# Optimization experiments

Measured on AMD Instinct MI355X. Metric: run time of the kernel, lower is better.

## Reference

```python
import jax, jax.numpy as jnp
import numpy as np

B, M, N, C = 1, 128, 256, 256
MID, OUT_C = 32, 128
LN_EPS = 1e-5
NORM_EPS = 1e-3


def setup_inputs() -> dict:
    key = jax.random.key(0)
    ks = jax.random.split(key, 9)
    act = jax.random.normal(ks[0], (B, M, N, C), dtype=jnp.float32)
    mask = (jax.random.uniform(ks[1], (B, M, N)) < 0.9).astype(jnp.float32)
    s_in = 1.0 / np.sqrt(C)
    s_mid = 1.0 / np.sqrt(MID * MID)
    return {
        "act": act,
        "mask": mask,
        "ln_g": jnp.ones((C,), jnp.float32),
        "ln_b": jnp.zeros((C,), jnp.float32),
        "lw": jax.random.normal(ks[2], (MID, C), jnp.float32) * s_in,
        "lb": jnp.zeros((MID,), jnp.float32),
        "rw": jax.random.normal(ks[3], (MID, C), jnp.float32) * s_in,
        "rb": jnp.zeros((MID,), jnp.float32),
        "ow": jax.random.normal(ks[4], (OUT_C, MID * MID), jnp.float32) * s_mid,
        "ob": jnp.zeros((OUT_C,), jnp.float32),
    }


def reference(act, mask, ln_g, ln_b, lw, lb, rw, rb, ow, ob):
    # LayerNorm over channel dim
    mu = jnp.mean(act, axis=-1, keepdims=True)
    var = jnp.mean(jnp.square(act - mu), axis=-1, keepdims=True)
    x = (act - mu) * jax.lax.rsqrt(var + LN_EPS) * ln_g + ln_b  # [b,m,i,c]

    m = mask[..., None]  # [b,m,i,1]
    left = m * (jnp.einsum('bmic,xc->bmix', x, lw) + lb)   # [b,m,i,mid]
    right = m * (jnp.einsum('bmic,yc->bmiy', x, rw) + rb)  # [b,m,i,mid]

    # outer product mean over MSA dim m -> [b,i,j,x,y]
    x2d = jnp.einsum('bmix,bmjy->bijxy', left, right)
    x2d = x2d.reshape(x2d.shape[:3] + (MID * MID,))
    out = jnp.einsum('bijk,ok->bijo', x2d, ow) + ob  # [b,i,j,out_c]

    norm = jnp.einsum('bmi,bmj->bij', mask, mask)[..., None]
    return out / (norm + NORM_EPS)
```

## Files before the change

kernel.cpp:

```cpp
#include <hip/hip_runtime.h>
#include <hip/hip_bf16.h>

typedef __bf16 bf16x8 __attribute__((ext_vector_type(8)));
typedef __bf16 bf16x4 __attribute__((ext_vector_type(4)));
typedef float  f32x4  __attribute__((ext_vector_type(4)));
typedef float  f32x16 __attribute__((ext_vector_type(16)));

#define MDIM 128
#define NDIM 256
#define CDIM 256
#define MIDC 32
#define OUTC 128

#define LSX_RS 1156
#define LSX_YS 36
#define LSX_BYTES (64 * LSX_RS * 2)

__global__ __launch_bounds__(256) void prep_kernel(
    const float* __restrict__ mask,
    const float* __restrict__ lw, const float* __restrict__ lb,
    const float* __restrict__ rw, const float* __restrict__ rb,
    const float* __restrict__ ow,
    __bf16* __restrict__ wb, float* __restrict__ cbias,
    __bf16* __restrict__ owb_f, float* __restrict__ norm_inv)
{
    int b = blockIdx.x, t = threadIdx.x;
    if (b < 256) {
        float s = 0.f;
        #pragma unroll 8
        for (int m = 0; m < MDIM; ++m)
            s += mask[m*NDIM + b] * mask[m*NDIM + t];
        norm_inv[b*NDIM + t] = 1.0f / (s + 1e-3f);
    } else if (b < 320) {
        int e0 = (b - 256)*2048 + t*8;
        #pragma unroll
        for (int jj = 0; jj < 8; ++jj) {
            int e = e0 + jj;
            int lane = (e >> 3) & 63;
            int s = (e >> 9) & 63;
            int ot = e >> 15;
            int o = ot*32 + (lane & 31);
            int x = (s & 1)*16 + (lane >> 5)*8 + jj;
            int y = s >> 1;
            owb_f[e] = (__bf16)ow[o*1024 + x*32 + y];
        }
    } else {
        int e0 = (b - 320)*2048 + t*8;
        #pragma unroll
        for (int j = 0; j < 8; ++j) {
            int e = e0 + j;
            int row = e >> 8, c = e & 255;
            wb[e] = (__bf16)(row < MIDC ? lw[row*CDIM + c] : rw[(row - MIDC)*CDIM + c]);
        }
        if (b == 320 && t < 64) cbias[t] = (t < MIDC) ? lb[t] : rb[t - MIDC];
    }
}

__global__ __launch_bounds__(256) void ln_proj_kernel(
    const float* __restrict__ act, const float* __restrict__ mask,
    const float* __restrict__ ln_g, const float* __restrict__ ln_b,
    const __bf16* __restrict__ wb, const float* __restrict__ cbias,
    __bf16* __restrict__ left_f, __bf16* __restrict__ right_f)
{
    __shared__ __bf16 xls[64][264];
    __shared__ __bf16 T[64][72];
    int t = threadIdx.x, lane = t & 63, w = t >> 6;
    int quad = lane >> 4, l16 = lane & 15;
    int b  = blockIdx.x;
    int m0 = blockIdx.y * 64;

    float4 gv = *(const float4*)(ln_g + lane*4);
    float4 bv = *(const float4*)(ln_b + lane*4);
    const float inv_c = 1.0f / 256.0f;

    #pragma unroll 4
    for (int s = 0; s < 16; ++s) {
        int m = m0 + w*16 + s;
        float4 v = *(const float4*)(act + ((size_t)m*NDIM + b)*CDIM + lane*4);
        float sum = v.x + v.y + v.z + v.w;
        float ssq = v.x*v.x + v.y*v.y + v.z*v.z + v.w*v.w;
        #pragma unroll
        for (int d = 1; d < 64; d <<= 1) {
            sum += __shfl_xor(sum, d);
            ssq += __shfl_xor(ssq, d);
        }
        float mu   = sum * inv_c;
        float var  = ssq * inv_c - mu*mu;
        float rstd = rsqrtf(var + 1e-5f);
        bf16x4 o;
        o.x = (__bf16)((v.x - mu)*rstd*gv.x + bv.x);
        o.y = (__bf16)((v.y - mu)*rstd*gv.y + bv.y);
        o.z = (__bf16)((v.z - mu)*rstd*gv.z + bv.z);
        o.w = (__bf16)((v.w - mu)*rstd*gv.w + bv.w);
        *(bf16x4*)&xls[w*16 + s][lane*4] = o;
    }

    f32x4 acc[4] = {};
    const __bf16* arow = &xls[w*16 + l16][0];
    #pragma unroll
    for (int k0 = 0; k0 < 256; k0 += 32) {
        bf16x8 a = *(const bf16x8*)(arow + k0 + quad*8);
        #pragma unroll
        for (int tt = 0; tt < 4; ++tt) {
            bf16x8 bb = *(const bf16x8*)(wb + (size_t)(tt*16 + l16)*CDIM + k0 + quad*8);
            acc[tt] = __builtin_amdgcn_mfma_f32_16x16x32_bf16(a, bb, acc[tt], 0, 0, 0);
        }
    }

    #pragma unroll
    for (int rg = 0; rg < 4; ++rg) {
        int ml = w*16 + quad*4 + rg;
        float mval = mask[(size_t)(m0 + ml)*NDIM + b];
        #pragma unroll
        for (int tt = 0; tt < 4; ++tt) {
            int o = tt*16 + l16;
            T[o][ml] = (__bf16)(mval * (acc[tt][rg] + cbias[o]));
        }
    }
    __syncthreads();

    {
        int fl16  = t & 15;
        int r     = t >> 4;
        int q     = r & 3;
        int k0loc = (r >> 2) & 1;
        int half  = (r >> 3) & 1;
        int tile  = b*2 + half;
        int k0    = (m0 >> 5) + k0loc;
        size_t dstoff = (((size_t)tile*4 + k0)*64 + q*16 + fl16)*8;
        #pragma unroll
        for (int side = 0; side < 2; ++side) {
            int o = side*32 + half*16 + fl16;
            bf16x8 d = *(const bf16x8*)&T[o][k0loc*32 + q*8];
            __bf16* dst = side ? right_f : left_f;
            *(bf16x8*)(dst + dstoff) = d;
        }
    }
}

__global__ __launch_bounds__(1024, 1) void outer_kernel(
    const __bf16* __restrict__ left_f, const __bf16* __restrict__ right_f,
    const __bf16* __restrict__ owb_f, const float* __restrict__ ob,
    const float* __restrict__ norm_inv, float* __restrict__ out)
{
    extern __shared__ __bf16 lsX[];
    int t = threadIdx.x, lane = t & 63, w = t >> 6;
    int quad = lane >> 4, l16 = lane & 15;
    int l31 = lane & 31, half = lane >> 5;

    int id = blockIdx.x;
    int xcd = id & 7, p = id >> 3;
    int bi = xcd*4 + (p & 3);
    int bj = p >> 2;

    {
        uint4* ls4 = (uint4*)lsX;
        const uint4* gA4 = (const uint4*)(left_f  + (size_t)bi*32768);
        const uint4* gB4 = (const uint4*)(right_f + (size_t)bj*32768);
        #pragma unroll
        for (int r = 0; r < 4; ++r) ls4[r*1024 + t]        = gA4[r*1024 + t];
        #pragma unroll
        for (int r = 0; r < 4; ++r) ls4[4096 + r*1024 + t] = gB4[r*1024 + t];
    }
    __syncthreads();

    int wr = w & 3, wc = w >> 2;
    const __bf16* lsA = lsX;
    const __bf16* lsB = lsX + 32768;

    f32x4 acc1[4][4] = {};
    #pragma unroll
    for (int kk = 0; kk < 4; ++kk) {
        bf16x8 af[4], bg[4];
        #pragma unroll
        for (int tr = 0; tr < 4; ++tr)
            af[tr] = *(const bf16x8*)(lsA + (size_t)(((wr*4 + tr)*4 + kk)*512) + lane*8);
        #pragma unroll
        for (int tc = 0; tc < 4; ++tc)
            bg[tc] = *(const bf16x8*)(lsB + (size_t)(((wc*4 + tc)*4 + kk)*512) + lane*8);
        #pragma unroll
        for (int tr = 0; tr < 4; ++tr)
            #pragma unroll
            for (int tc = 0; tc < 4; ++tc)
                acc1[tr][tc] = __builtin_amdgcn_mfma_f32_16x16x32_bf16(af[tr], bg[tc], acc1[tr][tc], 0, 0, 0);
    }

    int ot = w & 3, kq = w >> 2;
    const __bf16* Ob = owb_f + ((size_t)(ot*64 + kq*16)*64 + lane)*8;
    bf16x8 bbuf0 = *(const bf16x8*)(Ob);
    bf16x8 bbuf1 = *(const bf16x8*)(Ob + 512);

    __syncthreads();

    #pragma unroll
    for (int tr = 0; tr < 4; ++tr) {
        int il = wr*2 + (tr >> 1);
        int x0 = (tr & 1)*16 + quad*4;
        #pragma unroll
        for (int tc = 0; tc < 4; ++tc) {
            int jl = wc*2 + (tc >> 1);
            int y  = (tc & 1)*16 + l16;
            bf16x4 pk;
            pk.x = (__bf16)acc1[tr][tc][0];
            pk.y = (__bf16)acc1[tr][tc][1];
            pk.z = (__bf16)acc1[tr][tc][2];
            pk.w = (__bf16)acc1[tr][tc][3];
            *(bf16x4*)(lsX + (size_t)(il*8 + jl)*LSX_RS + y*LSX_YS + x0) = pk;
        }
    }
    __syncthreads();

    f32x16 acc2[2] = {};
    const __bf16* Xb = lsX + (size_t)l31*LSX_RS + half*8;
    #pragma unroll 4
    for (int ss = 0; ss < 16; ++ss) {
        int s = kq*16 + ss;
        bf16x8 bb = bbuf0;
        bbuf0 = bbuf1;
        if (ss + 2 < 16) bbuf1 = *(const bf16x8*)(Ob + (ss + 2)*512);
        int xoff = (s >> 1)*LSX_YS + (s & 1)*16;
        #pragma unroll
        for (int rt = 0; rt < 2; ++rt) {
            const __bf16* ap = Xb + (size_t)rt*32*LSX_RS + xoff;
            bf16x4 lo = *(const bf16x4*)(ap);
            bf16x4 hi = *(const bf16x4*)(ap + 4);
            bf16x8 a  = __builtin_shufflevector(lo, hi, 0, 1, 2, 3, 4, 5, 6, 7);
            acc2[rt] = __builtin_amdgcn_mfma_f32_32x32x16_bf16(a, bb, acc2[rt], 0, 0, 0);
        }
    }

    __syncthreads();

    float* scr = (float*)lsX;
    if (kq > 0) {
        int base = (kq - 1)*8192 + ot*2048;
        #pragma unroll
        for (int rt = 0; rt < 2; ++rt) {
            #pragma unroll
            for (int r = 0; r < 16; ++r) {
                int row = (r & 3) + 8*(r >> 2) + 4*half;
                scr[base + rt*1024 + row*32 + l31] = acc2[rt][r];
            }
        }
    }
    __syncthreads();

    if (kq == 0) {
        int o = ot*32 + l31;
        float obv = ob[o];
        #pragma unroll
        for (int rt = 0; rt < 2; ++rt) {
            #pragma unroll
            for (int r = 0; r < 16; ++r) {
                int row = (r & 3) + 8*(r >> 2) + 4*half;
                int idx = ot*2048 + rt*1024 + row*32 + l31;
                float v = acc2[rt][r] + scr[idx] + scr[8192 + idx] + scr[16384 + idx];
                int ij = rt*32 + row;
                int i = bi*8 + (ij >> 3), j = bj*8 + (ij & 7);
                out[((size_t)(i*NDIM + j))*OUTC + o] = (v + obv) * norm_inv[i*NDIM + j];
            }
        }
    }
}

extern "C" void kernel_launch(void* const* d_in, const int* in_sizes, int n_in,
                              void* d_out, int out_size, void* d_ws, size_t ws_size,
                              hipStream_t stream) {
    const float* act  = (const float*)d_in[0];
    const float* mask = (const float*)d_in[1];
    const float* ln_g = (const float*)d_in[2];
    const float* ln_b = (const float*)d_in[3];
    const float* lw   = (const float*)d_in[4];
    const float* lb   = (const float*)d_in[5];
    const float* rw   = (const float*)d_in[6];
    const float* rb   = (const float*)d_in[7];
    const float* ow   = (const float*)d_in[8];
    const float* ob   = (const float*)d_in[9];
    float* out = (float*)d_out;

    unsigned char* ws = (unsigned char*)d_ws;
    __bf16* left_f   = (__bf16*)(ws + 0);
    __bf16* right_f  = (__bf16*)(ws + (2u<<20));
    __bf16* owb_f    = (__bf16*)(ws + (4u<<20));
    float*  norm_inv = (float*) (ws + (4u<<20) + (256u<<10));
    __bf16* wb       = (__bf16*)(ws + (4u<<20) + (512u<<10));
    float*  cbias    = (float*) (ws + (4u<<20) + (544u<<10));

    hipFuncSetAttribute((const void*)outer_kernel,
                        hipFuncAttributeMaxDynamicSharedMemorySize, LSX_BYTES);

    prep_kernel<<<328, 256, 0, stream>>>(mask, lw, lb, rw, rb, ow,
                                         wb, cbias, owb_f, norm_inv);
    ln_proj_kernel<<<dim3(256, 2), 256, 0, stream>>>(act, mask, ln_g, ln_b,
                                                     wb, cbias, left_f, right_f);
    outer_kernel<<<1024, 1024, LSX_BYTES, stream>>>(left_f, right_f, owb_f, ob,
                                                    norm_inv, out);
}
```

Baseline: 153.3 us.

## Shrink outer-product blocks to 512 threads and read fragments from global

The outer kernel now runs 2048 blocks of 512 threads, each covering a 4x8 (i,j) tile instead of 8x8. Launch bounds allow several blocks per CU, and the LDS footprint is halved. The left/right MFMA fragments are read straight from global memory instead of being staged through LDS, which drops a barrier. The output-projection K dimension is split across two wave groups instead of four, so the cross-wave reduction is smaller. The aim is better occupancy and overlap of the two GEMM stages, at the cost of more redundant global/L2 reads of the fragments and the output weights.

Result: slower. 161.2 us (+5.2%).

```diff
diff --git a/kernel.cpp b/kernel.cpp
--- a/kernel.cpp
+++ b/kernel.cpp
@@ -14,7 +14,7 @@
 
 #define LSX_RS 1156
 #define LSX_YS 36
-#define LSX_BYTES (64 * LSX_RS * 2)
+#define LSX_BYTES (32 * LSX_RS * 2)
 
 __global__ __launch_bounds__(256) void prep_kernel(
     const float* __restrict__ mask,
@@ -138,7 +138,7 @@
     }
 }
 
-__global__ __launch_bounds__(1024, 1) void outer_kernel(
+__global__ __launch_bounds__(512, 4) void outer_kernel(
     const __bf16* __restrict__ left_f, const __bf16* __restrict__ right_f,
     const __bf16* __restrict__ owb_f, const float* __restrict__ ob,
     const float* __restrict__ norm_inv, float* __restrict__ out)
@@ -150,34 +150,21 @@
 
     int id = blockIdx.x;
     int xcd = id & 7, p = id >> 3;
-    int bi = xcd*4 + (p & 3);
-    int bj = p >> 2;
-
-    {
-        uint4* ls4 = (uint4*)lsX;
-        const uint4* gA4 = (const uint4*)(left_f  + (size_t)bi*32768);
-        const uint4* gB4 = (const uint4*)(right_f + (size_t)bj*32768);
-        #pragma unroll
-        for (int r = 0; r < 4; ++r) ls4[r*1024 + t]        = gA4[r*1024 + t];
-        #pragma unroll
-        for (int r = 0; r < 4; ++r) ls4[4096 + r*1024 + t] = gB4[r*1024 + t];
-    }
-    __syncthreads();
-
-    int wr = w & 3, wc = w >> 2;
-    const __bf16* lsA = lsX;
-    const __bf16* lsB = lsX + 32768;
+    int bi = xcd*8 + (p & 7);
+    int bj = p >> 3;
+
+    int wr = w & 1, wc = w >> 1;
+    const __bf16* Af = left_f  + ((size_t)(bi*8  + wr*4)*4)*512 + lane*8;
+    const __bf16* Bf = right_f + ((size_t)(bj*16 + wc*4)*4)*512 + lane*8;
 
     f32x4 acc1[4][4] = {};
     #pragma unroll
     for (int kk = 0; kk < 4; ++kk) {
         bf16x8 af[4], bg[4];
         #pragma unroll
-        for (int tr = 0; tr < 4; ++tr)
-            af[tr] = *(const bf16x8*)(lsA + (size_t)(((wr*4 + tr)*4 + kk)*512) + lane*8);
-        #pragma unroll
-        for (int tc = 0; tc < 4; ++tc)
-            bg[tc] = *(const bf16x8*)(lsB + (size_t)(((wc*4 + tc)*4 + kk)*512) + lane*8);
+        for (int tr = 0; tr < 4; ++tr) af[tr] = *(const bf16x8*)(Af + tr*2048 + kk*512);
+        #pragma unroll
+        for (int tc = 0; tc < 4; ++tc) bg[tc] = *(const bf16x8*)(Bf + tc*2048 + kk*512);
         #pragma unroll
         for (int tr = 0; tr < 4; ++tr)
             #pragma unroll
@@ -185,12 +172,10 @@
                 acc1[tr][tc] = __builtin_amdgcn_mfma_f32_16x16x32_bf16(af[tr], bg[tc], acc1[tr][tc], 0, 0, 0);
     }
 
-    int ot = w & 3, kq = w >> 2;
-    const __bf16* Ob = owb_f + ((size_t)(ot*64 + kq*16)*64 + lane)*8;
+    int ot = w & 3, kh = w >> 2;
+    const __bf16* Ob = owb_f + ((size_t)(ot*64 + kh*32)*64 + lane)*8;
     bf16x8 bbuf0 = *(const bf16x8*)(Ob);
     bf16x8 bbuf1 = *(const bf16x8*)(Ob + 512);
-
-    __syncthreads();
 
     #pragma unroll
     for (int tr = 0; tr < 4; ++tr) {
@@ -210,55 +195,43 @@
     }
     __syncthreads();
 
-    f32x16 acc2[2] = {};
+    f32x16 acc2 = {};
     const __bf16* Xb = lsX + (size_t)l31*LSX_RS + half*8;
     #pragma unroll 4
-    for (int ss = 0; ss < 16; ++ss) {
-        int s = kq*16 + ss;
+    for (int ss = 0; ss < 32; ++ss) {
+        int s = kh*32 + ss;
         bf16x8 bb = bbuf0;
         bbuf0 = bbuf1;
-        if (ss + 2 < 16) bbuf1 = *(const bf16x8*)(Ob + (ss + 2)*512);
+        if (ss + 2 < 32) bbuf1 = *(const bf16x8*)(Ob + (ss + 2)*512);
         int xoff = (s >> 1)*LSX_YS + (s & 1)*16;
-        #pragma unroll
-        for (int rt = 0; rt < 2; ++rt) {
-            const __bf16* ap = Xb + (size_t)rt*32*LSX_RS + xoff;
-            bf16x4 lo = *(const bf16x4*)(ap);
-            bf16x4 hi = *(const bf16x4*)(ap + 4);
-            bf16x8 a  = __builtin_shufflevector(lo, hi, 0, 1, 2, 3, 4, 5, 6, 7);
-            acc2[rt] = __builtin_amdgcn_mfma_f32_32x32x16_bf16(a, bb, acc2[rt], 0, 0, 0);
-        }
-    }
-
+        const __bf16* ap = Xb + xoff;
+        bf16x4 lo = *(const bf16x4*)(ap);
+        bf16x4 hi = *(const bf16x4*)(ap + 4);
+        bf16x8 a  = __builtin_shufflevector(lo, hi, 0, 1, 2, 3, 4, 5, 6, 7);
+        acc2 = __builtin_amdgcn_mfma_f32_32x32x16_bf16(a, bb, acc2, 0, 0, 0);
+    }
     __syncthreads();
 
     float* scr = (float*)lsX;
-    if (kq > 0) {
-        int base = (kq - 1)*8192 + ot*2048;
-        #pragma unroll
-        for (int rt = 0; rt < 2; ++rt) {
-            #pragma unroll
-            for (int r = 0; r < 16; ++r) {
-                int row = (r & 3) + 8*(r >> 2) + 4*half;
-                scr[base + rt*1024 + row*32 + l31] = acc2[rt][r];
-            }
-        }
-    }
-    __syncthreads();
-
-    if (kq == 0) {
+    if (kh == 1) {
+        int base = ot*1024;
+        #pragma unroll
+        for (int r = 0; r < 16; ++r) {
+            int row = (r & 3) + 8*(r >> 2) + 4*half;
+            scr[base + row*32 + l31] = acc2[r];
+        }
+    }
+    __syncthreads();
+
+    if (kh == 0) {
         int o = ot*32 + l31;
         float obv = ob[o];
         #pragma unroll
-        for (int rt = 0; rt < 2; ++rt) {
-            #pragma unroll
-            for (int r = 0; r < 16; ++r) {
-                int row = (r & 3) + 8*(r >> 2) + 4*half;
-                int idx = ot*2048 + rt*1024 + row*32 + l31;
-                float v = acc2[rt][r] + scr[idx] + scr[8192 + idx] + scr[16384 + idx];
-                int ij = rt*32 + row;
-                int i = bi*8 + (ij >> 3), j = bj*8 + (ij & 7);
-                out[((size_t)(i*NDIM + j))*OUTC + o] = (v + obv) * norm_inv[i*NDIM + j];
-            }
+        for (int r = 0; r < 16; ++r) {
+            int row = (r & 3) + 8*(r >> 2) + 4*half;
+            float v = acc2[r] + scr[ot*1024 + row*32 + l31];
+            int i = bi*4 + (row >> 3), j = bj*8 + (row & 7);
+            out[((size_t)(i*NDIM + j))*OUTC + o] = (v + obv) * norm_inv[i*NDIM + j];
         }
     }
 }
@@ -293,6 +266,6 @@
                                          wb, cbias, owb_f, norm_inv);
     ln_proj_kernel<<<dim3(256, 2), 256, 0, stream>>>(act, mask, ln_g, ln_b,
                                                      wb, cbias, left_f, right_f);
-    outer_kernel<<<1024, 1024, LSX_BYTES, stream>>>(left_f, right_f, owb_f, ob,
-                                                    norm_inv, out);
-}
+    outer_kernel<<<2048, 512, LSX_BYTES, stream>>>(left_f, right_f, owb_f, ob,
+                                                   norm_inv, out);
+}
```
